# Kernel tuning notes

Measured on AMD Instinct MI355X. Metric: run time of the kernel, lower is better.

Reference implementation:

```python
import jax, jax.numpy as jnp
import numpy as np

EPS = 1.0        # model eps for norm
STEP = 0.05      # step_size

def _norm(x):
    # torch: x / (eps + x.std(-1, keepdims=True)), torch std is unbiased (ddof=1)
    return x / (EPS + jnp.std(x, axis=-1, keepdims=True, ddof=1))

def setup_inputs() -> dict:
    key = jax.random.key(0)
    B, L, LM = 4, 512, 64
    G, E, K, D, KN = 32000, 256, 8, 6, 4
    ks = jax.random.split(key, 16)
    s = lambda k, shape, fan: (jax.random.normal(k, shape, jnp.float32) / np.sqrt(fan)).astype(jnp.float32)
    return dict(
        masked=jax.random.randint(ks[0], (B, L), 0, G),
        unmasked=jax.random.randint(ks[1], (B, L), 0, G),
        mask=jax.random.randint(ks[2], (B, LM), 0, L),
        embed=s(ks[3], (G, E), E),                 # embedding table
        Wt=s(ks[4], (D, E, E), E),                 # transition.weight per layer
        bt=jnp.zeros((D, E), jnp.float32),         # transition.bias per layer
        Wtc=s(ks[5], (D, E, E), E),                # transcore.weight per layer
        Wq=s(ks[6], (D, K * E, E), E),             # attq.weight per layer
        Wd=s(ks[7], (D, K * E, K * E), K * E),     # att_dense.weight per layer
        Wo=s(ks[8], (D, K * E, E), K * E),         # atto.weight per layer
        Wu=s(ks[9], (D, E, E), E),                 # updater.weight per layer
        Wem=s(ks[10], (E, E), E),                  # emittor.weight (head)
        Wkc=s(ks[11], (E * KN, E), E),             # kchoice.weight (head)
        bkc=jnp.zeros((E * KN,), jnp.float32),     # kchoice.bias (head)
    )

def reference(masked, unmasked, mask, embed, Wt, bt, Wtc, Wq, Wd, Wo, Wu, Wem, Wkc, bkc):
    B, L = masked.shape
    G, E = embed.shape
    K = Wq.shape[1] // E
    KN = Wkc.shape[0] // E
    inv_sqrt_e = 1.0 / np.sqrt(E)

    z = _norm(embed[masked])          # [B,L,E] input image
    xsa0 = z

    def step(xsa, p):
        wt, bt_, wtc, wq, wd, wo, wu = p
        # roll-based left/right transitions
        xsad = jax.nn.relu(jnp.roll(xsa, 1, axis=1) @ wt) @ wtc
        xsad = xsad + jax.nn.relu(jnp.roll(xsa, -1, axis=1) @ wtc.T) @ wt.T
        xsad = xsad + z @ wu.T + bt_   # use_input_image
        # QKV_Attention with kernel-expanded head dim: q [B,L,K,E] vs keys/values xsa [B,L,E]
        q = (xsa @ wq.T).reshape(B, L, K, E)
        h = jnp.einsum('blke,bme->blkm', q, xsa) * inv_sqrt_e
        pijk = jax.nn.softmax(h, axis=-1)
        y = jnp.einsum('blkm,bme->blke', pijk, xsa).reshape(B, L, K * E)
        # mode 1: Dense -> Relu -> Dense
        xid = jax.nn.relu(y @ wd.T) @ wo     # [B,L,E]
        xsad = _norm(xsad + xid)             # use_gradnorm
        xsa = _norm(xsa + STEP * xsad)       # use_layernorm
        return xsa, None

    xsa, _ = jax.lax.scan(step, xsa0, (Wt, bt, Wtc, Wq, Wd, Wo, Wu))

    # k-choice loss head (callback_cent)
    LM = mask.shape[1]
    lptok = jnp.take_along_axis(xsa, mask[:, :, None], axis=1)         # [B,LM,E]
    xx = (lptok @ Wkc.T + bkc).reshape(B, LM * KN, E)                  # kchoice
    xx = jnp.einsum('bnl,ble->bne', jnp.einsum('bne,ble->bnl', xx, xsa), xsa)
    logits = (xx @ Wem) @ embed.T                                      # [B,LM*KN,G]
    k_lp = jax.nn.log_softmax(logits, axis=-1).reshape(B, LM, KN, G)
    lptok = jax.scipy.special.logsumexp(k_lp, axis=2) - jnp.log(jnp.float32(KN))
    tgt = jnp.take_along_axis(unmasked, mask, axis=1)                  # [B,LM]
    cent = jnp.take_along_axis(lptok, tgt[:, :, None], axis=-1)[:, :, 0]
    return -cent.mean(-1)                                              # [B]
```

## Files before the change

### kernel.cpp

```cpp
#include <hip/hip_runtime.h>
#include <hip/hip_bf16.h>
#include <math.h>

typedef __bf16 bf16x8 __attribute__((ext_vector_type(8)));
typedef float floatx4 __attribute__((ext_vector_type(4)));

__device__ __forceinline__ short f2b(float f) {
  __hip_bfloat16 h = __float2bfloat16(f);
  return *reinterpret_cast<short*>(&h);
}
__device__ __forceinline__ float b2f(short s) {
  unsigned u = ((unsigned)(unsigned short)s) << 16;
  float f;
  __builtin_memcpy(&f, &u, 4);
  return f;
}

__device__ __forceinline__ void gl2lds16(const void* g, void* l) {
  __builtin_amdgcn_global_load_lds((__attribute__((address_space(1))) const void*)g,
                                   (__attribute__((address_space(3))) void*)l, 16, 0, 0);
}

__device__ __forceinline__ float block_sum(float v, float* sdata) {
#pragma unroll
  for (int o = 32; o > 0; o >>= 1) v += __shfl_down(v, o, 64);
  __syncthreads();
  int lane = threadIdx.x & 63, wid = threadIdx.x >> 6;
  if (lane == 0) sdata[wid] = v;
  __syncthreads();
  float s = 0.f;
  int nw = blockDim.x >> 6;
  for (int i = 0; i < nw; i++) s += sdata[i];
  return s;
}

__global__ void cvt_kernel(const float* __restrict__ src, short* __restrict__ dst, long n4) {
  long i = (long)blockIdx.x * blockDim.x + threadIdx.x;
  if (i < n4) {
    float4 v = ((const float4*)src)[i];
    short4 o;
    o.x = f2b(v.x); o.y = f2b(v.y); o.z = f2b(v.z); o.w = f2b(v.w);
    ((short4*)dst)[i] = o;
  }
}

__global__ void cvt2_kernel(const float* __restrict__ src, short* __restrict__ dst,
                            int ldS, int ldD, long sS, long sD) {
  src += (size_t)blockIdx.z * sS;
  dst += (size_t)blockIdx.z * sD;
  int c = blockIdx.x * 32 + threadIdx.x;
  int r0 = blockIdx.y * 32 + threadIdx.y;
#pragma unroll
  for (int i = 0; i < 32; i += 8)
    dst[(size_t)(r0 + i) * ldD + c] = f2b(src[(size_t)(r0 + i) * ldS + c]);
}

__global__ void cvtT2_kernel(const float* __restrict__ src, short* __restrict__ dst,
                             int ldS, int ldD, long sS, long sD) {
  src += (size_t)blockIdx.z * sS;
  dst += (size_t)blockIdx.z * sD;
  __shared__ float tile[32][33];
  int r0 = blockIdx.y * 32, c0 = blockIdx.x * 32;
  int tx = threadIdx.x, ty = threadIdx.y;
#pragma unroll
  for (int i = 0; i < 32; i += 8)
    tile[ty + i][tx] = src[(size_t)(r0 + ty + i) * ldS + c0 + tx];
  __syncthreads();
#pragma unroll
  for (int i = 0; i < 32; i += 8)
    dst[(size_t)(c0 + ty + i) * ldD + r0 + tx] = f2b(tile[tx][ty + i]);
}

__global__ void embed_norm_kernel(const int* __restrict__ masked,
                                  const float* __restrict__ embed,
                                  float* __restrict__ xsa, short* __restrict__ xsa_bf,
                                  short* __restrict__ xsaT_bf, short* __restrict__ t3,
                                  int E, int L) {
  int row = blockIdx.x;
  int g = masked[row];
  __shared__ float sdata[8];
  float x = embed[(size_t)g * E + threadIdx.x];
  float mean = block_sum(x, sdata) / E;
  float d = x - mean;
  float var = block_sum(d * d, sdata) / (E - 1);
  float val = x / (1.0f + sqrtf(var));
  size_t off = (size_t)row * E + threadIdx.x;
  xsa[off] = val;
  short b = f2b(val);
  xsa_bf[off] = b;
  t3[(size_t)row * 3 * E + 2 * E + threadIdx.x] = b;
  int bb = row / L, l = row - bb * L;
  xsaT_bf[((size_t)bb * E + threadIdx.x) * L + l] = b;
}

template <int BM, int BN, int OUT_BF16>
__global__ __launch_bounds__(256) void bgemm_kernel(
    const short* __restrict__ A, int lda, long sA,
    const short* __restrict__ B, int ldb, long sB,
    void* __restrict__ Cv, int ldc, long sC,
    int Ksz, float alpha, const float* __restrict__ bias,
    int relu, int shiftA, int shiftB, int nsplit, int Lroll) {
  constexpr int WM = BM / 2, WN = BN / 2;
  constexpr int MT = WM / 16, NT = WN / 16;
  constexpr int NCH = (BM + BN) * 8;
  constexpr int LPT = NCH / 256;
  A += (size_t)blockIdx.z * sA;
  B += (size_t)blockIdx.z * sB;
  float* Cf = (float*)Cv + (size_t)blockIdx.z * sC;
  short* Cb = (short*)Cv + (size_t)blockIdx.z * sC;
  int m0 = blockIdx.y * BM, n0 = blockIdx.x * BN;
  int shift = (n0 < nsplit) ? shiftA : shiftB;
  __shared__ short S[2][(BM + BN) * 64];
  int tid = threadIdx.x, lane = tid & 63, w = tid >> 6;
  int wm = (w & 1) * WM, wn = (w >> 1) * WN;
  int ml = lane & 15, q4 = lane >> 4, sw = ml & 7;

  const short* src[LPT];
#pragma unroll
  for (int i = 0; i < LPT; i++) {
    int q = i * 256 + w * 64 + lane;
    if (q < BM * 8) {
      int m = q >> 3, cl = q & 7, cs = cl ^ (m & 7);
      int mg = m0 + m;
      if (shift != 0) {
        int bb = mg / Lroll, l = mg - bb * Lroll;
        l = (l + shift + Lroll) % Lroll;
        mg = bb * Lroll + l;
      }
      src[i] = A + (size_t)mg * lda + cs * 8;
    } else {
      int qb = q - BM * 8;
      int n = qb >> 3, cl = qb & 7, cs = cl ^ (n & 7);
      src[i] = B + (size_t)(n0 + n) * ldb + cs * 8;
    }
  }
#pragma unroll
  for (int i = 0; i < LPT; i++)
    gl2lds16(src[i], &S[0][(i * 256 + w * 64) * 8]);
  floatx4 acc[MT][NT] = {};
  int nT = Ksz >> 6;
  for (int t = 0; t < nT; t++) {
    __syncthreads();
    int cur = t & 1;
    if (t + 1 < nT) {
      int nxt = cur ^ 1, ko = (t + 1) * 64;
#pragma unroll
      for (int i = 0; i < LPT; i++)
        gl2lds16(src[i] + ko, &S[nxt][(i * 256 + w * 64) * 8]);
    }
#pragma unroll
    for (int kk = 0; kk < 2; kk++) {
      int j = kk * 4 + q4;
      bf16x8 af[MT], bg[NT];
#pragma unroll
      for (int mt = 0; mt < MT; mt++) {
        int r = wm + mt * 16 + ml;
        af[mt] = *reinterpret_cast<const bf16x8*>(&S[cur][r * 64 + (j ^ sw) * 8]);
      }
#pragma unroll
      for (int nt = 0; nt < NT; nt++) {
        int r = wn + nt * 16 + ml;
        bg[nt] = *reinterpret_cast<const bf16x8*>(&S[cur][BM * 64 + r * 64 + (j ^ sw) * 8]);
      }
#pragma unroll
      for (int mt = 0; mt < MT; mt++)
#pragma unroll
        for (int nt = 0; nt < NT; nt++)
          acc[mt][nt] = __builtin_amdgcn_mfma_f32_16x16x32_bf16(af[mt], bg[nt], acc[mt][nt], 0, 0, 0);
    }
  }
#pragma unroll
  for (int mt = 0; mt < MT; mt++)
#pragma unroll
    for (int nt = 0; nt < NT; nt++) {
      floatx4 v = acc[mt][nt];
#pragma unroll
      for (int r = 0; r < 4; r++) {
        int grow = m0 + wm + mt * 16 + q4 * 4 + r;
        int gcol = n0 + wn + nt * 16 + ml;
        float x = alpha * v[r];
        if (bias) x += bias[gcol];
        if (relu) x = fmaxf(x, 0.f);
        if (OUT_BF16)
          Cb[(size_t)grow * ldc + gcol] = f2b(x);
        else
          Cf[(size_t)grow * ldc + gcol] = x;
      }
    }
}

__global__ void softmax_bf_kernel(short* __restrict__ h) {
  int lane = threadIdx.x & 63;
  size_t row = (size_t)blockIdx.x * 4 + (threadIdx.x >> 6);
  short* p = h + row * 512 + lane * 8;
  int4 raw = *(const int4*)p;
  short sh[8];
  __builtin_memcpy(sh, &raw, 16);
  float v[8];
  float m = -INFINITY;
#pragma unroll
  for (int i = 0; i < 8; i++) {
    v[i] = b2f(sh[i]);
    m = fmaxf(m, v[i]);
  }
#pragma unroll
  for (int o = 1; o < 64; o <<= 1) m = fmaxf(m, __shfl_xor(m, o, 64));
  float s = 0.f;
#pragma unroll
  for (int i = 0; i < 8; i++) {
    v[i] = expf(v[i] - m);
    s += v[i];
  }
#pragma unroll
  for (int o = 1; o < 64; o <<= 1) s += __shfl_xor(s, o, 64);
  float inv = 1.f / s;
#pragma unroll
  for (int i = 0; i < 8; i++) sh[i] = f2b(v[i] * inv);
  __builtin_memcpy(&raw, sh, 16);
  *(int4*)p = raw;
}

__global__ void addnorm_kernel(const float* __restrict__ xsad,
                               const float* __restrict__ xid,
                               float* __restrict__ xsa, short* __restrict__ xsa_bf,
                               short* __restrict__ xsaT_bf, int E, int L) {
  int row = blockIdx.x, t = threadIdx.x;
  __shared__ float sdata[8];
  size_t off = (size_t)row * E + t;
  float s1 = xsad[off] + xid[off];
  float mean = block_sum(s1, sdata) / E;
  float d = s1 - mean;
  float var = block_sum(d * d, sdata) / (E - 1);
  float n1 = s1 / (1.f + sqrtf(var));
  float t2 = xsa[off] + 0.05f * n1;
  float mean2 = block_sum(t2, sdata) / E;
  float d2 = t2 - mean2;
  float var2 = block_sum(d2 * d2, sdata) / (E - 1);
  float res = t2 / (1.f + sqrtf(var2));
  xsa[off] = res;
  short b = f2b(res);
  xsa_bf[off] = b;
  int bb = row / L, l = row - bb * L;
  xsaT_bf[((size_t)bb * E + t) * L + l] = b;
}

__global__ void gather_kernel(const float* __restrict__ xsa, const int* __restrict__ mask,
                              const int* __restrict__ unmasked,
                              short* __restrict__ lptok_bf, int* __restrict__ tgt,
                              int L, int LM, int E) {
  int bi = blockIdx.x;
  int b = bi / LM;
  int pos = mask[bi];
  float v = xsa[((size_t)b * L + pos) * E + threadIdx.x];
  lptok_bf[(size_t)bi * E + threadIdx.x] = f2b(v);
  if (threadIdx.x == 0) tgt[bi] = unmasked[b * L + pos];
}

__global__ __launch_bounds__(256) void head_stats_kernel(
    const short* __restrict__ V, const short* __restrict__ Eb,
    float* __restrict__ stM, float* __restrict__ stS, int Ksz, int nch) {
  int m0 = blockIdx.y * 128, n0 = blockIdx.x * 128;
  __shared__ short As[2][8192];
  __shared__ short Bs[2][8192];
  int tid = threadIdx.x, lane = tid & 63, w = tid >> 6;
  int wm = (w & 1) * 64, wn = (w >> 1) * 64;
  int ml = lane & 15, q4 = lane >> 4, sw = ml & 7;
  const short* aSrc[4];
  const short* bSrc[4];
#pragma unroll
  for (int i = 0; i < 4; i++) {
    int q = i * 256 + w * 64 + lane;
    int m = q >> 3, cl = q & 7;
    int cs = cl ^ (m & 7);
    aSrc[i] = V + (size_t)(m0 + m) * Ksz + cs * 8;
    bSrc[i] = Eb + (size_t)(n0 + m) * Ksz + cs * 8;
  }
#pragma unroll
  for (int i = 0; i < 4; i++) {
    gl2lds16(aSrc[i], &As[0][(i * 256 + w * 64) * 8]);
    gl2lds16(bSrc[i], &Bs[0][(i * 256 + w * 64) * 8]);
  }
  floatx4 acc[4][4] = {};
  int nT = Ksz >> 6;
  for (int t = 0; t < nT; t++) {
    __syncthreads();
    int cur = t & 1;
    if (t + 1 < nT) {
      int nxt = cur ^ 1, ko = (t + 1) * 64;
#pragma unroll
      for (int i = 0; i < 4; i++) {
        gl2lds16(aSrc[i] + ko, &As[nxt][(i * 256 + w * 64) * 8]);
        gl2lds16(bSrc[i] + ko, &Bs[nxt][(i * 256 + w * 64) * 8]);
      }
    }
#pragma unroll
    for (int kk = 0; kk < 2; kk++) {
      int j = kk * 4 + q4;
      bf16x8 af[4], bg[4];
#pragma unroll
      for (int mt = 0; mt < 4; mt++) {
        int r = wm + mt * 16 + ml;
        af[mt] = *reinterpret_cast<const bf16x8*>(&As[cur][r * 64 + (j ^ sw) * 8]);
      }
#pragma unroll
      for (int nt = 0; nt < 4; nt++) {
        int r = wn + nt * 16 + ml;
        bg[nt] = *reinterpret_cast<const bf16x8*>(&Bs[cur][r * 64 + (j ^ sw) * 8]);
      }
#pragma unroll
      for (int mt = 0; mt < 4; mt++)
#pragma unroll
        for (int nt = 0; nt < 4; nt++)
          acc[mt][nt] = __builtin_amdgcn_mfma_f32_16x16x32_bf16(af[mt], bg[nt], acc[mt][nt], 0, 0, 0);
    }
  }
  __syncthreads();
  float (*sred)[2] = (float (*)[2]) & As[0][0];
  float (*sred2)[2] = (float (*)[2]) & Bs[0][0];
  float mx[4][4];
#pragma unroll
  for (int mt = 0; mt < 4; mt++)
#pragma unroll
    for (int r = 0; r < 4; r++)
      mx[mt][r] = fmaxf(fmaxf(acc[mt][0][r], acc[mt][1][r]), fmaxf(acc[mt][2][r], acc[mt][3][r]));
#pragma unroll
  for (int off = 1; off < 16; off <<= 1)
#pragma unroll
    for (int mt = 0; mt < 4; mt++)
#pragma unroll
      for (int r = 0; r < 4; r++) mx[mt][r] = fmaxf(mx[mt][r], __shfl_xor(mx[mt][r], off, 64));
  if (ml == 0)
#pragma unroll
    for (int mt = 0; mt < 4; mt++)
#pragma unroll
      for (int r = 0; r < 4; r++) sred[wm + mt * 16 + q4 * 4 + r][w >> 1] = mx[mt][r];
  __syncthreads();
  float sm[4][4];
#pragma unroll
  for (int mt = 0; mt < 4; mt++)
#pragma unroll
    for (int r = 0; r < 4; r++) {
      int row = wm + mt * 16 + q4 * 4 + r;
      float fm = fmaxf(sred[row][0], sred[row][1]);
      float s = 0.f;
#pragma unroll
      for (int nt = 0; nt < 4; nt++) s += expf(acc[mt][nt][r] - fm);
      sm[mt][r] = s;
    }
#pragma unroll
  for (int off = 1; off < 16; off <<= 1)
#pragma unroll
    for (int mt = 0; mt < 4; mt++)
#pragma unroll
      for (int r = 0; r < 4; r++) sm[mt][r] += __shfl_xor(sm[mt][r], off, 64);
  if (ml == 0)
#pragma unroll
    for (int mt = 0; mt < 4; mt++)
#pragma unroll
      for (int r = 0; r < 4; r++) sred2[wm + mt * 16 + q4 * 4 + r][w >> 1] = sm[mt][r];
  __syncthreads();
  if (tid < 128) {
    float fm = fmaxf(sred[tid][0], sred[tid][1]);
    stM[(size_t)(m0 + tid) * nch + blockIdx.x] = fm;
    stS[(size_t)(m0 + tid) * nch + blockIdx.x] = sred2[tid][0] + sred2[tid][1];
  }
}

__global__ void lse_reduce_kernel(const float* __restrict__ statsM,
                                  const float* __restrict__ statsS,
                                  float* __restrict__ lse, int nch) {
  int row = blockIdx.x, t = threadIdx.x;
  float m = -INFINITY, s = 0.f;
  for (int c = t; c < nch; c += blockDim.x) {
    float cm = statsM[(size_t)row * nch + c];
    float cs = statsS[(size_t)row * nch + c];
    float M = fmaxf(m, cm);
    s = s * expf(m - M) + cs * expf(cm - M);
    m = M;
  }
  __shared__ float sm[256], ss[256];
  sm[t] = m;
  ss[t] = s;
  __syncthreads();
  for (int o = 128; o > 0; o >>= 1) {
    if (t < o) {
      float m2 = sm[t + o], s2 = ss[t + o];
      float M = fmaxf(sm[t], m2);
      float sc = ss[t] * expf(sm[t] - M) + s2 * expf(m2 - M);
      sm[t] = M;
      ss[t] = sc;
    }
    __syncthreads();
  }
  if (t == 0) lse[row] = sm[0] + logf(ss[0]);
}

__global__ void logit_tgt_kernel(const short* __restrict__ V, const short* __restrict__ Eb,
                                 const int* __restrict__ tgt, float* __restrict__ lt,
                                 int E, int Nn, int KN, int LM) {
  int row = blockIdx.x;
  int b = row / Nn;
  int i = (row - b * Nn) / KN;
  int g = tgt[b * LM + i];
  __shared__ float sdata[8];
  float v = b2f(V[(size_t)row * E + threadIdx.x]) * b2f(Eb[(size_t)g * E + threadIdx.x]);
  float s = block_sum(v, sdata);
  if (threadIdx.x == 0) lt[row] = s;
}

__global__ void final_kernel(const float* __restrict__ lt, const float* __restrict__ lse,
                             float* __restrict__ out, int LM, int KN) {
  int b = blockIdx.x, i = threadIdx.x;
  int base = (b * LM + i) * KN;
  float m = -INFINITY;
  for (int k = 0; k < KN; k++) m = fmaxf(m, lt[base + k] - lse[base + k]);
  float s = 0.f;
  for (int k = 0; k < KN; k++) s += expf(lt[base + k] - lse[base + k] - m);
  float cent = m + logf(s) - logf((float)KN);
#pragma unroll
  for (int o = 32; o > 0; o >>= 1) cent += __shfl_down(cent, o, 64);
  if (i == 0) out[b] = -cent / LM;
}

static inline void bgemm(hipStream_t st, int cfg, const short* A, int lda, long sA,
                         const short* B, int ldb, long sB,
                         void* C, int ldc, long sC, int M, int N, int Ksz, int nb,
                         float alpha, const float* bias, int relu, int out_bf16,
                         int shiftA, int shiftB, int nsplit, int Lroll) {
  dim3 block(256);
  if (cfg == 0) {
    dim3 grid(N / 128, M / 128, nb);
    if (out_bf16)
      bgemm_kernel<128, 128, 1><<<grid, block, 0, st>>>(A, lda, sA, B, ldb, sB, C, ldc, sC, Ksz, alpha, bias, relu, shiftA, shiftB, nsplit, Lroll);
    else
      bgemm_kernel<128, 128, 0><<<grid, block, 0, st>>>(A, lda, sA, B, ldb, sB, C, ldc, sC, Ksz, alpha, bias, relu, shiftA, shiftB, nsplit, Lroll);
  } else if (cfg == 1) {
    dim3 grid(N / 64, M / 128, nb);
    if (out_bf16)
      bgemm_kernel<128, 64, 1><<<grid, block, 0, st>>>(A, lda, sA, B, ldb, sB, C, ldc, sC, Ksz, alpha, bias, relu, shiftA, shiftB, nsplit, Lroll);
    else
      bgemm_kernel<128, 64, 0><<<grid, block, 0, st>>>(A, lda, sA, B, ldb, sB, C, ldc, sC, Ksz, alpha, bias, relu, shiftA, shiftB, nsplit, Lroll);
  } else {
    dim3 grid(N / 64, M / 64, nb);
    if (out_bf16)
      bgemm_kernel<64, 64, 1><<<grid, block, 0, st>>>(A, lda, sA, B, ldb, sB, C, ldc, sC, Ksz, alpha, bias, relu, shiftA, shiftB, nsplit, Lroll);
    else
      bgemm_kernel<64, 64, 0><<<grid, block, 0, st>>>(A, lda, sA, B, ldb, sB, C, ldc, sC, Ksz, alpha, bias, relu, shiftA, shiftB, nsplit, Lroll);
  }
}

static inline void cvt(hipStream_t st, const float* src, short* dst, long n) {
  long n4 = n / 4;
  cvt_kernel<<<(int)((n4 + 255) / 256), 256, 0, st>>>(src, dst, n4);
}

static inline void cvt2(hipStream_t st, const float* src, short* dst, int R, int C,
                        int ldS, int ldD, long sS, long sD, int nb) {
  dim3 grid(C / 32, R / 32, nb), block(32, 8);
  cvt2_kernel<<<grid, block, 0, st>>>(src, dst, ldS, ldD, sS, sD);
}

static inline void cvtT2(hipStream_t st, const float* src, short* dst, int R, int C,
                         int ldS, int ldD, long sS, long sD, int nb) {
  dim3 grid(C / 32, R / 32, nb), block(32, 8);
  cvtT2_kernel<<<grid, block, 0, st>>>(src, dst, ldS, ldD, sS, sD);
}

extern "C" void kernel_launch(void* const* d_in, const int* in_sizes, int n_in,
                              void* d_out, int out_size, void* d_ws, size_t ws_size,
                              hipStream_t stream) {
  const int* masked = (const int*)d_in[0];
  const int* unmasked = (const int*)d_in[1];
  const int* mask = (const int*)d_in[2];
  const float* embed = (const float*)d_in[3];
  const float* Wt = (const float*)d_in[4];
  const float* bt = (const float*)d_in[5];
  const float* Wtc = (const float*)d_in[6];
  const float* Wq = (const float*)d_in[7];
  const float* Wd = (const float*)d_in[8];
  const float* Wo = (const float*)d_in[9];
  const float* Wu = (const float*)d_in[10];
  const float* Wem = (const float*)d_in[11];
  const float* Wkc = (const float*)d_in[12];
  const float* bkc = (const float*)d_in[13];

  const int B = out_size;
  const int BL = in_sizes[0];
  const int L = BL / B;
  const int BLM = in_sizes[2];
  const int LM = BLM / B;
  const int E = in_sizes[4] / in_sizes[5];
  const int D = in_sizes[5] / E;
  const int G = in_sizes[3] / E;
  const int K = in_sizes[7] / (D * E * E);
  const int KN = in_sizes[12] / (E * E);
  const int KE = K * E;
  const int N = LM * KN;
  const float inv_sqrt_e = 1.0f / sqrtf((float)E);
  const int nch = G / 128;
  const int E3 = 3 * E;

  char* base = (char*)d_ws;
  size_t off = 0;
  auto carve = [&](size_t bytes) {
    char* p = base + off;
    off += (bytes + 255) & ~(size_t)255;
    return p;
  };
  float* xsa = (float*)carve((size_t)BL * E * 4);
  float* xsad = (float*)carve((size_t)BL * E * 4);
  float* xid = (float*)carve((size_t)BL * E * 4);
  float* stM = (float*)carve((size_t)B * N * nch * 4);
  float* stS = (float*)carve((size_t)B * N * nch * 4);
  float* lse = (float*)carve((size_t)B * N * 4);
  float* lt = (float*)carve((size_t)B * N * 4);
  int* tgt = (int*)carve((size_t)B * LM * 4);
  short* xsa_bf = (short*)carve((size_t)BL * E * 2);
  short* xsaT_bf = (short*)carve((size_t)B * E * L * 2);
  short* t3 = (short*)carve((size_t)BL * E3 * 2);
  short* qy_bf = (short*)carve((size_t)BL * KE * 2);
  short* hP_bf = (short*)carve((size_t)B * L * K * L * 2);
  short* r_bf = hP_bf;
  short* wd_all = (short*)carve((size_t)D * KE * KE * 2);
  short* wq_all = (short*)carve((size_t)D * KE * E * 2);
  short* woT_all = (short*)carve((size_t)D * E * KE * 2);
  short* Bcat1 = (short*)carve((size_t)D * 2 * E * E * 2);
  short* Bcat2 = (short*)carve((size_t)D * E * E3 * 2);
  short* embed_bf = (short*)carve((size_t)G * E * 2);
  short* WemT_bf = (short*)carve((size_t)E * E * 2);
  short* Wkc_bf = (short*)carve((size_t)KN * E * E * 2);
  short* gram_bf = (short*)carve((size_t)B * E * E * 2);
  short* xx_bf = (short*)carve((size_t)B * N * E * 2);
  short* xx2_bf = (short*)carve((size_t)B * N * E * 2);
  short* vv_bf = (short*)carve((size_t)B * N * E * 2);
  short* lptok_bf = (short*)carve((size_t)BLM * E * 2);

  cvt(stream, embed, embed_bf, (long)G * E);
  cvt(stream, Wd, wd_all, (long)D * KE * KE);
  cvt(stream, Wq, wq_all, (long)D * KE * E);
  cvt(stream, Wkc, Wkc_bf, (long)KN * E * E);
  cvtT2(stream, Wem, WemT_bf, E, E, E, E, 0, 0, 1);
  cvtT2(stream, Wo, woT_all, KE, E, E, KE, (long)KE * E, (long)E * KE, D);
  cvtT2(stream, Wt, Bcat1, E, E, E, E, (long)E * E, (long)2 * E * E, D);
  cvt2(stream, Wtc, Bcat1 + (size_t)E * E, E, E, E, E, (long)E * E, (long)2 * E * E, D);
  cvtT2(stream, Wtc, Bcat2, E, E, E, E3, (long)E * E, (long)E * E3, D);
  cvt2(stream, Wt, Bcat2 + E, E, E, E, E3, (long)E * E, (long)E * E3, D);
  cvt2(stream, Wu, Bcat2 + 2 * E, E, E, E, E3, (long)E * E, (long)E * E3, D);

  embed_norm_kernel<<<BL, E, 0, stream>>>(masked, embed, xsa, xsa_bf, xsaT_bf, t3, E, L);

  for (int d = 0; d < D; d++) {
    const float* btl = bt + (size_t)d * E;
    bgemm(stream, 2, xsa_bf, E, 0, Bcat1 + (size_t)d * 2 * E * E, E, 0,
          t3, E3, 0, BL, 2 * E, E, 1, 1.f, nullptr, 1, 1, -1, +1, E, L);
    bgemm(stream, 2, t3, E3, 0, Bcat2 + (size_t)d * E * E3, E3, 0,
          xsad, E, 0, BL, E, E3, 1, 1.f, btl, 0, 0, 0, 0, 0, L);
    bgemm(stream, 1, xsa_bf, E, 0, wq_all + (size_t)d * KE * E, E, 0,
          qy_bf, KE, 0, BL, KE, E, 1, 1.f, nullptr, 0, 1, 0, 0, 0, L);
    bgemm(stream, 0, qy_bf, E, (long)L * KE, xsa_bf, E, (long)L * E,
          hP_bf, L, (long)L * K * L, L * K, L, E, B, inv_sqrt_e, nullptr, 0, 1, 0, 0, 0, L);
    softmax_bf_kernel<<<B * L * K / 4, 256, 0, stream>>>(hP_bf);
    bgemm(stream, 1, hP_bf, L, (long)L * K * L, xsaT_bf, L, (long)E * L,
          qy_bf, E, (long)L * KE, L * K, E, L, B, 1.f, nullptr, 0, 1, 0, 0, 0, L);
    bgemm(stream, 1, qy_bf, KE, 0, wd_all + (size_t)d * KE * KE, KE, 0,
          r_bf, KE, 0, BL, KE, KE, 1, 1.f, nullptr, 1, 1, 0, 0, 0, L);
    bgemm(stream, 2, r_bf, KE, 0, woT_all + (size_t)d * E * KE, KE, 0,
          xid, E, 0, BL, E, KE, 1, 1.f, nullptr, 0, 0, 0, 0, 0, L);
    addnorm_kernel<<<BL, E, 0, stream>>>(xsad, xid, xsa, xsa_bf, xsaT_bf, E, L);
  }

  gather_kernel<<<BLM, E, 0, stream>>>(xsa, mask, unmasked, lptok_bf, tgt, L, LM, E);
  bgemm(stream, 2, xsaT_bf, L, (long)E * L, xsaT_bf, L, (long)E * L,
        gram_bf, E, (long)E * E, E, E, L, B, 1.f, nullptr, 0, 1, 0, 0, 0, L);
  bgemm(stream, 2, lptok_bf, E, 0, Wkc_bf, E, 0, xx_bf, KN * E, 0, BLM, KN * E, E, 1,
        1.f, bkc, 0, 1, 0, 0, 0, L);
  bgemm(stream, 2, xx_bf, E, (long)N * E, gram_bf, E, (long)E * E,
        xx2_bf, E, (long)N * E, N, E, E, B, 1.f, nullptr, 0, 1, 0, 0, 0, L);
  bgemm(stream, 2, xx2_bf, E, 0, WemT_bf, E, 0, vv_bf, E, 0, B * N, E, E, 1,
        1.f, nullptr, 0, 1, 0, 0, 0, L);
  head_stats_kernel<<<dim3(nch, (B * N) / 128), 256, 0, stream>>>(vv_bf, embed_bf, stM, stS, E, nch);
  lse_reduce_kernel<<<B * N, 256, 0, stream>>>(stM, stS, lse, nch);
  logit_tgt_kernel<<<B * N, E, 0, stream>>>(vv_bf, embed_bf, tgt, lt, E, N, KN, LM);
  final_kernel<<<B, LM, 0, stream>>>(lt, lse, (float*)d_out, LM, KN);
}
```

Baseline: 949.1 us.

## Fuse attention score GEMM, softmax and value GEMM into one kernel

Replaces the QK^T GEMM, the separate bf16 softmax pass and the PV GEMM with a single attention kernel. Each block handles 32 query rows over the full 512-key length, keeps scores in registers, does the softmax with LDS-based cross-wave reductions, then multiplies by V with double-buffered LDS loads. This removes the round trip of the large B*L*K*L score matrix through global memory and two kernel launches per layer. In exchange, each block uses 64 KB of LDS and many registers, which may limit occupancy, and the output is written in place over qy.

```diff
diff --git a/kernel.cpp b/kernel.cpp
--- a/kernel.cpp
+++ b/kernel.cpp
@@ -189,35 +189,144 @@
     }
 }
 
-__global__ void softmax_bf_kernel(short* __restrict__ h) {
-  int lane = threadIdx.x & 63;
-  size_t row = (size_t)blockIdx.x * 4 + (threadIdx.x >> 6);
-  short* p = h + row * 512 + lane * 8;
-  int4 raw = *(const int4*)p;
-  short sh[8];
-  __builtin_memcpy(sh, &raw, 16);
-  float v[8];
-  float m = -INFINITY;
+__global__ __launch_bounds__(256) void attn_kernel(short* __restrict__ qy,
+                                                   const short* __restrict__ kbf,
+                                                   const short* __restrict__ vtbf,
+                                                   float scale) {
+  constexpr int L = 512, E = 256;
+  int b = blockIdx.y;
+  int m0 = blockIdx.x * 32;
+  short* Qg = qy + ((size_t)b * 4096 + m0) * E;
+  const short* Kg = kbf + (size_t)b * L * E;
+  const short* Vt = vtbf + (size_t)b * E * L;
+  __shared__ short LDS[32768];
+  int tid = threadIdx.x, lane = tid & 63, w = tid >> 6;
+  int ml = lane & 15, q4 = lane >> 4;
+  int wm = (w & 1) * 16, wh = w >> 1;
+  int wn1 = wh * 256;
+  int wn2 = wh * 128;
+
+  bf16x8 af_q[8];
+  {
+    const short* qsrc = Qg + (size_t)(wm + ml) * E + q4 * 8;
+#pragma unroll
+    for (int kt = 0; kt < 8; kt++)
+      af_q[kt] = *reinterpret_cast<const bf16x8*>(qsrc + kt * 32);
+  }
+
+  const short* srcB[8];
 #pragma unroll
   for (int i = 0; i < 8; i++) {
-    v[i] = b2f(sh[i]);
-    m = fmaxf(m, v[i]);
-  }
-#pragma unroll
-  for (int o = 1; o < 64; o <<= 1) m = fmaxf(m, __shfl_xor(m, o, 64));
-  float s = 0.f;
-#pragma unroll
-  for (int i = 0; i < 8; i++) {
-    v[i] = expf(v[i] - m);
-    s += v[i];
-  }
-#pragma unroll
-  for (int o = 1; o < 64; o <<= 1) s += __shfl_xor(s, o, 64);
-  float inv = 1.f / s;
-#pragma unroll
-  for (int i = 0; i < 8; i++) sh[i] = f2b(v[i] * inv);
-  __builtin_memcpy(&raw, sh, 16);
-  *(int4*)p = raw;
+    int idx = i * 256 + tid;
+    srcB[i] = Kg + (size_t)(idx & 511) * E + (idx >> 9) * 8;
+  }
+#pragma unroll
+  for (int i = 0; i < 8; i++)
+    gl2lds16(srcB[i], &LDS[(i * 256 + w * 64) * 8]);
+
+  floatx4 sacc[16] = {};
+  for (int kt = 0; kt < 8; kt++) {
+    __syncthreads();
+    int cur = kt & 1;
+    if (kt + 1 < 8) {
+      int nxt = cur ^ 1, ko = (kt + 1) * 32;
+#pragma unroll
+      for (int i = 0; i < 8; i++)
+        gl2lds16(srcB[i] + ko, &LDS[nxt * 16384 + (i * 256 + w * 64) * 8]);
+    }
+    const short* bb = &LDS[cur * 16384];
+    bf16x8 a = af_q[kt];
+#pragma unroll
+    for (int nt = 0; nt < 16; nt++) {
+      bf16x8 bg = *reinterpret_cast<const bf16x8*>(bb + (q4 * 512 + wn1 + nt * 16 + ml) * 8);
+      sacc[nt] = __builtin_amdgcn_mfma_f32_16x16x32_bf16(a, bg, sacc[nt], 0, 0, 0);
+    }
+  }
+  __syncthreads();
+
+  const short* srcV[4];
+#pragma unroll
+  for (int i = 0; i < 4; i++) srcV[i] = Vt + (size_t)tid * L + i * 8;
+#pragma unroll
+  for (int i = 0; i < 4; i++)
+    gl2lds16(srcV[i], &LDS[16384 + (i * 256 + w * 64) * 8]);
+
+  float mrow[4] = {-INFINITY, -INFINITY, -INFINITY, -INFINITY};
+#pragma unroll
+  for (int nt = 0; nt < 16; nt++)
+#pragma unroll
+    for (int r = 0; r < 4; r++) {
+      float v = sacc[nt][r] * scale;
+      sacc[nt][r] = v;
+      mrow[r] = fmaxf(mrow[r], v);
+    }
+#pragma unroll
+  for (int o = 1; o < 16; o <<= 1)
+#pragma unroll
+    for (int r = 0; r < 4; r++) mrow[r] = fmaxf(mrow[r], __shfl_xor(mrow[r], o, 64));
+  float* stM = (float*)&LDS[24576];
+  float* stS = stM + 64;
+  if (ml == 0)
+#pragma unroll
+    for (int r = 0; r < 4; r++) stM[wh * 32 + wm + q4 * 4 + r] = mrow[r];
+  __syncthreads();
+  float fm[4], ps[4] = {0.f, 0.f, 0.f, 0.f};
+#pragma unroll
+  for (int r = 0; r < 4; r++)
+    fm[r] = fmaxf(stM[wm + q4 * 4 + r], stM[32 + wm + q4 * 4 + r]);
+#pragma unroll
+  for (int nt = 0; nt < 16; nt++)
+#pragma unroll
+    for (int r = 0; r < 4; r++) {
+      float p = expf(sacc[nt][r] - fm[r]);
+      sacc[nt][r] = p;
+      ps[r] += p;
+    }
+#pragma unroll
+  for (int o = 1; o < 16; o <<= 1)
+#pragma unroll
+    for (int r = 0; r < 4; r++) ps[r] += __shfl_xor(ps[r], o, 64);
+  if (ml == 0)
+#pragma unroll
+    for (int r = 0; r < 4; r++) stS[wh * 32 + wm + q4 * 4 + r] = ps[r];
+  __syncthreads();
+  float inv[4];
+#pragma unroll
+  for (int r = 0; r < 4; r++)
+    inv[r] = 1.f / (stS[wm + q4 * 4 + r] + stS[32 + wm + q4 * 4 + r]);
+
+#pragma unroll
+  for (int nt = 0; nt < 16; nt++) {
+    int n = wn1 + nt * 16 + ml;
+    int base = ((n >> 3) * 32) * 8 + (n & 7);
+#pragma unroll
+    for (int r = 0; r < 4; r++)
+      LDS[base + (wm + q4 * 4 + r) * 8] = f2b(sacc[nt][r] * inv[r]);
+  }
+
+  floatx4 oacc[8] = {};
+  for (int kc = 0; kc < 16; kc++) {
+    __syncthreads();
+    int cur = kc & 1;
+    if (kc + 1 < 16) {
+      int nxt = cur ^ 1, ko = (kc + 1) * 32;
+#pragma unroll
+      for (int i = 0; i < 4; i++)
+        gl2lds16(srcV[i] + ko, &LDS[16384 + nxt * 8192 + (i * 256 + w * 64) * 8]);
+    }
+    bf16x8 ap = *reinterpret_cast<const bf16x8*>(&LDS[((kc * 4 + q4) * 32 + wm + ml) * 8]);
+    const short* vb = &LDS[16384 + cur * 8192];
+#pragma unroll
+    for (int nt = 0; nt < 8; nt++) {
+      bf16x8 bg = *reinterpret_cast<const bf16x8*>(vb + (q4 * 256 + wn2 + nt * 16 + ml) * 8);
+      oacc[nt] = __builtin_amdgcn_mfma_f32_16x16x32_bf16(ap, bg, oacc[nt], 0, 0, 0);
+    }
+  }
+#pragma unroll
+  for (int nt = 0; nt < 8; nt++)
+#pragma unroll
+    for (int r = 0; r < 4; r++)
+      Qg[(size_t)(wm + q4 * 4 + r) * E + wn2 + nt * 16 + ml] = f2b(oacc[nt][r]);
 }
 
 __global__ void addnorm_kernel(const float* __restrict__ xsad,
@@ -519,8 +628,7 @@
   short* xsaT_bf = (short*)carve((size_t)B * E * L * 2);
   short* t3 = (short*)carve((size_t)BL * E3 * 2);
   short* qy_bf = (short*)carve((size_t)BL * KE * 2);
-  short* hP_bf = (short*)carve((size_t)B * L * K * L * 2);
-  short* r_bf = hP_bf;
+  short* r_bf = (short*)carve((size_t)B * L * K * L * 2);
   short* wd_all = (short*)carve((size_t)D * KE * KE * 2);
   short* wq_all = (short*)carve((size_t)D * KE * E * 2);
   short* woT_all = (short*)carve((size_t)D * E * KE * 2);
@@ -557,11 +665,7 @@
           xsad, E, 0, BL, E, E3, 1, 1.f, btl, 0, 0, 0, 0, 0, L);
     bgemm(stream, 1, xsa_bf, E, 0, wq_all + (size_t)d * KE * E, E, 0,
           qy_bf, KE, 0, BL, KE, E, 1, 1.f, nullptr, 0, 1, 0, 0, 0, L);
-    bgemm(stream, 0, qy_bf, E, (long)L * KE, xsa_bf, E, (long)L * E,
-          hP_bf, L, (long)L * K * L, L * K, L, E, B, inv_sqrt_e, nullptr, 0, 1, 0, 0, 0, L);
-    softmax_bf_kernel<<<B * L * K / 4, 256, 0, stream>>>(hP_bf);
-    bgemm(stream, 1, hP_bf, L, (long)L * K * L, xsaT_bf, L, (long)E * L,
-          qy_bf, E, (long)L * KE, L * K, E, L, B, 1.f, nullptr, 0, 1, 0, 0, 0, L);
+    attn_kernel<<<dim3(L * K / 32, B), 256, 0, stream>>>(qy_bf, xsa_bf, xsaT_bf, inv_sqrt_e);
     bgemm(stream, 1, qy_bf, KE, 0, wd_all + (size_t)d * KE * KE, KE, 0,
           r_bf, KE, 0, BL, KE, KE, 1, 1.f, nullptr, 1, 1, 0, 0, 0, L);
     bgemm(stream, 2, r_bf, KE, 0, woT_all + (size_t)d * E * KE, KE, 0,
```

Result: slower. 1.073 ms (+13.1%).
